# Performance work log

Measured on AMD Instinct MI355X. Metric: run time of the kernel, lower is better.

The kernel has to match this reference:

```python
import jax, jax.numpy as jnp
from jax import lax
import numpy as np

# dims
B, S, IN, E = 2, 2048, 512, 1024
INNER = 2 * E              # mLSTM up-projection, proj_factor = 2.0
NH = 4                     # mLSTM cell heads
DH = INNER // NH           # 512
QKV_BLK = 4                # qkv_proj_blocksize
NHW = INNER // QKV_BLK     # heads of block-diagonal (headwise) q/k/v projections
K = 4                      # causal conv1d kernel size
EPS = 1e-6                 # mLSTM cell eps
LN_EPS = 1e-5


def setup_inputs() -> dict:
    key = jax.random.key(0)
    ks = jax.random.split(key, 16)
    n = lambda k, shp, s=0.02: jax.random.normal(k, shp, jnp.float32) * s
    z = lambda shp: jnp.zeros(shp, jnp.float32)
    return dict(
        x=jax.random.normal(ks[0], (B, S, IN), jnp.float32),
        w_in=n(ks[1], (IN, E)), b_in=z((E,)),
        ln1_w=jnp.ones((E,), jnp.float32),
        w_up=n(ks[2], (E, 2 * INNER)), b_up=z((2 * INNER,)),
        conv_w=n(ks[3], (INNER, K), 0.1), conv_b=z((INNER,)),
        q_w=n(ks[4], (NHW, QKV_BLK, QKV_BLK), 0.3), q_b=z((INNER,)),
        k_w=n(ks[5], (NHW, QKV_BLK, QKV_BLK), 0.3), k_b=z((INNER,)),
        v_w=n(ks[6], (NHW, QKV_BLK, QKV_BLK), 0.3), v_b=z((INNER,)),
        ig_w=n(ks[7], (3 * INNER, NH)), ig_b=z((NH,)),
        fg_w=n(ks[8], (3 * INNER, NH)), fg_b=jnp.ones((NH,), jnp.float32),
        onorm_w=jnp.ones((INNER,), jnp.float32),
        skip=n(ks[9], (INNER,), 1.0),
        w_down=n(ks[10], (INNER, E)), b_down=z((E,)),
        post_w=jnp.ones((E,), jnp.float32),
    )


def _layernorm(x, w, eps=LN_EPS):
    m = x.mean(-1, keepdims=True)
    v = x.var(-1, keepdims=True)
    return (x - m) / jnp.sqrt(v + eps) * w


def _headwise(x, w, b):
    # block-diagonal linear: x (B,S,INNER) split into NHW blocks of QKV_BLK
    Bx, Sx, _ = x.shape
    y = jnp.einsum('bshd,hod->bsho', x.reshape(Bx, Sx, NHW, QKV_BLK), w)
    return y.reshape(Bx, Sx, INNER) + b


def _mlstm_parallel(q, k, v, ig, fg):
    # q,k,v: (B,NH,S,DH); ig,fg: (B,NH,S). Parallel (stabilized) mLSTM.
    log_f = jax.nn.log_sigmoid(fg)                       # (B,NH,S)
    cum = jnp.cumsum(log_f, axis=-1)                     # inclusive cumsum
    dmat = cum[..., :, None] - cum[..., None, :]         # F_i - F_j  (B,NH,S,S)
    mask = jnp.tril(jnp.ones((S, S), bool))
    logD = jnp.where(mask, dmat + ig[..., None, :], -jnp.inf)
    m = logD.max(-1, keepdims=True)                      # (B,NH,S,1)
    Dm = jnp.exp(logD - m)
    qk = jnp.einsum('bnid,bnjd->bnij', q, k) / jnp.sqrt(jnp.float32(DH))
    C = qk * Dm
    norm = jnp.maximum(jnp.abs(C.sum(-1, keepdims=True)), jnp.exp(-m))
    return jnp.einsum('bnij,bnjd->bnid', C / (norm + EPS), v)


def _forward(x, w_in, b_in, ln1_w, w_up, b_up, conv_w, conv_b,
             q_w, q_b, k_w, k_b, v_w, v_b, ig_w, ig_b, fg_w, fg_b,
             onorm_w, skip, w_down, b_down, post_w):
    h_in = x @ w_in + b_in                               # (B,S,E); dropout = identity (eval)

    # --- mLSTM block: residual + pre-LN ---
    xn = _layernorm(h_in, ln1_w)
    up = xn @ w_up + b_up                                # (B,S,2*INNER)
    x_m, z = jnp.split(up, 2, axis=-1)

    # causal depthwise conv1d + SiLU
    rhs = conv_w.T[:, None, :]                           # (K,1,INNER)
    xc = lax.conv_general_dilated(x_m, rhs, window_strides=(1,),
                                  padding=[(K - 1, 0)],
                                  dimension_numbers=('NHC', 'HIO', 'NHC'),
                                  feature_group_count=INNER) + conv_b
    x_conv_act = jax.nn.silu(xc)

    q = _headwise(x_conv_act, q_w, q_b)                  # (B,S,INNER)
    k = _headwise(x_conv_act, k_w, k_b)
    v = _headwise(x_m, v_w, v_b)

    if_in = jnp.concatenate([q, k, v], axis=-1)          # (B,S,3*INNER)
    ig = (if_in @ ig_w + ig_b).transpose(0, 2, 1)        # (B,NH,S)
    fg = (if_in @ fg_w + fg_b).transpose(0, 2, 1)

    to_heads = lambda t: t.reshape(B, S, NH, DH).transpose(0, 2, 1, 3)
    h = _mlstm_parallel(to_heads(q), to_heads(k), to_heads(v), ig, fg)  # (B,NH,S,DH)

    # multi-head (group) norm over DH, then learned scale over flat features
    hn = (h - h.mean(-1, keepdims=True)) / jnp.sqrt(h.var(-1, keepdims=True) + LN_EPS)
    hn = hn.transpose(0, 2, 1, 3).reshape(B, S, INNER) * onorm_w

    h_skip = hn + skip * x_conv_act                      # learnable skip
    h_gated = h_skip * jax.nn.silu(z)                    # output gate
    y = h_gated @ w_down + b_down                        # (B,S,E)

    out = h_in + y                                       # residual
    return _layernorm(out, post_w)                       # post_blocks_norm


def reference(x, w_in, b_in, ln1_w, w_up, b_up, conv_w, conv_b,
              q_w, q_b, k_w, k_b, v_w, v_b, ig_w, ig_b, fg_w, fg_b,
              onorm_w, skip, w_down, b_down, post_w):
    return _forward(x, w_in, b_in, ln1_w, w_up, b_up, conv_w, conv_b,
                    q_w, q_b, k_w, k_b, v_w, v_b, ig_w, ig_b, fg_w, fg_b,
                    onorm_w, skip, w_down, b_down, post_w)
```

## Files before the change

kernel.cpp:

```cpp
#include <hip/hip_runtime.h>
#include <hip/hip_bf16.h>

typedef __hip_bfloat16 bf16;
typedef float floatx4 __attribute__((ext_vector_type(4)));
typedef short bf16x8 __attribute__((ext_vector_type(8)));

#define B_      2
#define S_      2048
#define IN_     512
#define E_      1024
#define INNER_  2048
#define NH_     4
#define DH_     512
#define T_      (B_*S_)
#define EPS_CELL 1e-6f
#define LN_EPS_  1e-5f
#define LS      72
#define CTB_    4

__device__ inline float b2f(bf16 x){ return __bfloat162float(x); }
__device__ inline bf16  f2b(float x){ return __float2bfloat16(x); }
__device__ inline float us2f(unsigned short u){ union{unsigned int i; float f;} v; v.i = ((unsigned int)u)<<16; return v.f; }
__device__ inline float u2f(unsigned int u){ union{unsigned int i; float f;} v; v.i = u; return v.f; }
__device__ inline unsigned short f2bu(float x){ bf16 t = __float2bfloat16(x); unsigned short r; __builtin_memcpy(&r,&t,2); return r; }
__device__ inline void unpack8(uint4 u, float* f){
  f[0]=u2f(u.x<<16); f[1]=u2f(u.x&0xffff0000u);
  f[2]=u2f(u.y<<16); f[3]=u2f(u.y&0xffff0000u);
  f[4]=u2f(u.z<<16); f[5]=u2f(u.z&0xffff0000u);
  f[6]=u2f(u.w<<16); f[7]=u2f(u.w&0xffff0000u);
}
__device__ inline uint4 pack8(const float* f){
  uint4 u;
  u.x = (unsigned)f2bu(f[0]) | ((unsigned)f2bu(f[1])<<16);
  u.y = (unsigned)f2bu(f[2]) | ((unsigned)f2bu(f[3])<<16);
  u.z = (unsigned)f2bu(f[4]) | ((unsigned)f2bu(f[5])<<16);
  u.w = (unsigned)f2bu(f[6]) | ((unsigned)f2bu(f[7])<<16);
  return u;
}
__device__ inline void stv(bf16* p, float v){ *p = f2b(v); }
__device__ inline void stv(float* p, float v){ *p = v; }

typedef __attribute__((address_space(3))) unsigned int lds_u32_t;
typedef __attribute__((address_space(1))) const unsigned int glb_u32_t;
__device__ __forceinline__ void cp_async16(const bf16* g, short* l){
  __builtin_amdgcn_global_load_lds((glb_u32_t*)(const void*)g,
                                   (lds_u32_t*)(void*)l, 16, 0, 0);
}
__device__ __forceinline__ int so_(int row, int c8){ return row*64 + (((c8) ^ (row&7))<<3); }
__device__ __forceinline__ int eo_(int row, int ch){ return row*128 + (((ch) ^ (row&15))<<3); }

#define STAGE_ASYNC(dst, srcbase, stride, kk) \
  { int slot_ = (kk)*256 + tid; int r_ = slot_>>3; int c8_ = (slot_&7) ^ (r_&7); \
    cp_async16((srcbase) + (size_t)r_*(stride) + c8_*8, &dst[slot_*8]); }

__global__ __launch_bounds__(256) void convert_bf16(const float* __restrict__ X,
    bf16* __restrict__ Y, int n8){
  int i = blockIdx.x*256 + threadIdx.x;
  if (i >= n8) return;
  const float4* p = (const float4*)(X) + i*2;
  float4 a = p[0], b = p[1];
  ushort4 o0, o1;
  o0.x=f2bu(a.x); o0.y=f2bu(a.y); o0.z=f2bu(a.z); o0.w=f2bu(a.w);
  o1.x=f2bu(b.x); o1.y=f2bu(b.y); o1.z=f2bu(b.z); o1.w=f2bu(b.w);
  ushort4* q = (ushort4*)(Y) + i*2;
  q[0]=o0; q[1]=o1;
}

__global__ __launch_bounds__(256) void transpose_conv_w(const float* __restrict__ W,
    bf16* __restrict__ Wt, int K, int N){
  int n0 = blockIdx.x*64, k0 = blockIdx.y*64;
  __shared__ float tl[64][65];
  int tid = threadIdx.x;
  #pragma unroll
  for (int i=0;i<4;i++){
    int idx = tid + i*256; int r = idx>>4, c4 = idx&15;
    float4 v = *(const float4*)(W + (size_t)(k0+r)*N + n0 + c4*4);
    tl[r][c4*4+0]=v.x; tl[r][c4*4+1]=v.y; tl[r][c4*4+2]=v.z; tl[r][c4*4+3]=v.w;
  }
  __syncthreads();
  #pragma unroll
  for (int i=0;i<4;i++){
    int idx = tid + i*256; int rn = idx>>4, c4 = idx&15;
    ushort4 o;
    o.x=f2bu(tl[c4*4+0][rn]); o.y=f2bu(tl[c4*4+1][rn]);
    o.z=f2bu(tl[c4*4+2][rn]); o.w=f2bu(tl[c4*4+3][rn]);
    *(ushort4*)(Wt + (size_t)(n0+rn)*K + k0 + c4*4) = o;
  }
}

__global__ __launch_bounds__(256) void mfma_gemm(const bf16* __restrict__ A,
    const bf16* __restrict__ Bt, const float* __restrict__ bias, bf16* __restrict__ C,
    int Kd, int lda, int ldc, int NN){
  int bid = blockIdx.x;
  int MM = gridDim.x / NN;
  int mPerX = MM >> 3;
  int xcd = bid & 7, seq = bid >> 3;
  int nb = seq % NN, mb = xcd*mPerX + seq / NN;
  int n0 = nb*128, m0 = mb*128;
  __shared__ __align__(16) short smem[128*128];
  short* As = smem;
  short* Bs = smem + 128*64;
  int tid = threadIdx.x;
  int w = tid>>6, l = tid&63, lq = l>>4, lr = l&15;
  int wm = (w>>1)*64, wn = (w&1)*64;
  const bf16* Abase = A + (size_t)m0*lda;
  const bf16* Bbase = Bt + (size_t)n0*Kd;
  floatx4 acc[4][4];
  #pragma unroll
  for (int mi=0;mi<4;mi++){
    #pragma unroll
    for (int ni=0;ni<4;ni++) acc[mi][ni] = (floatx4){0.f,0.f,0.f,0.f};
  }
  for (int k0=0; k0<Kd; k0+=64){
    __syncthreads();
    #pragma unroll
    for (int kk=0;kk<4;kk++){
      STAGE_ASYNC(As, Abase + k0, lda, kk);
      STAGE_ASYNC(Bs, Bbase + k0, Kd, kk);
    }
    __syncthreads();
    #pragma unroll
    for (int ks=0; ks<2; ks++){
      bf16x8 af[4], bfr[4];
      #pragma unroll
      for (int mi=0;mi<4;mi++) af[mi] = *(const bf16x8*)&As[so_(wm+mi*16+lr, ks*4+lq)];
      #pragma unroll
      for (int ni=0;ni<4;ni++) bfr[ni] = *(const bf16x8*)&Bs[so_(wn+ni*16+lr, ks*4+lq)];
      #pragma unroll
      for (int mi=0;mi<4;mi++){
        #pragma unroll
        for (int ni=0;ni<4;ni++)
          acc[mi][ni] = __builtin_amdgcn_mfma_f32_16x16x32_bf16(af[mi], bfr[ni], acc[mi][ni], 0,0,0);
      }
    }
  }
  float bb[4];
  #pragma unroll
  for (int ni=0;ni<4;ni++) bb[ni] = bias[n0 + wn + ni*16 + lr];
  __syncthreads();
  #pragma unroll
  for (int mi=0;mi<4;mi++){
    #pragma unroll
    for (int ni=0;ni<4;ni++){
      int coll = wn + ni*16 + lr;
      int ch = coll>>3, off = coll&7;
      #pragma unroll
      for (int r=0;r<4;r++){
        int rowl = wm + mi*16 + lq*4 + r;
        smem[rowl*128 + (((ch) ^ (rowl&15))<<3) + off] = (short)f2bu(acc[mi][ni][r] + bb[ni]);
      }
    }
  }
  __syncthreads();
  #pragma unroll
  for (int i=0;i<8;i++){
    int slot = i*256 + tid;
    int r = slot >> 4, c8 = slot & 15;
    uint4 val = *(const uint4*)&smem[eo_(r, c8)];
    *(uint4*)(C + (size_t)(m0+r)*ldc + n0 + c8*8) = val;
  }
}

template<typename OutT>
__global__ __launch_bounds__(256) void ln_rows(const bf16* __restrict__ X,
    const bf16* __restrict__ Xadd, const float* __restrict__ w, OutT* __restrict__ Y){
  int row = blockIdx.x, tid = threadIdx.x;
  size_t base = (size_t)row*E_;
  float vals[4], s=0.f, s2=0.f;
  #pragma unroll
  for (int e=0;e<4;e++){
    int c = e*256+tid;
    float v = b2f(X[base+c]);
    if (Xadd) v += b2f(Xadd[base+c]);
    vals[e]=v; s+=v; s2+=v*v;
  }
  __shared__ float sa[256], sb[256];
  sa[tid]=s; sb[tid]=s2; __syncthreads();
  for (int off=128; off>0; off>>=1){
    if (tid<off){ sa[tid]+=sa[tid+off]; sb[tid]+=sb[tid+off]; }
    __syncthreads();
  }
  float mean = sa[0]*(1.f/E_);
  float var  = sb[0]*(1.f/E_) - mean*mean;
  float rstd = rsqrtf(var + LN_EPS_);
  #pragma unroll
  for (int e=0;e<4;e++){
    int c = e*256+tid;
    stv(&Y[base+c], (vals[e]-mean)*rstd*w[c]);
  }
}

__global__ __launch_bounds__(256) void conv_headwise(const bf16* __restrict__ up,
    const float* __restrict__ cw, const float* __restrict__ cb,
    const float* __restrict__ qw, const float* __restrict__ qb,
    const float* __restrict__ kw, const float* __restrict__ kb,
    const float* __restrict__ vw, const float* __restrict__ vb,
    bf16* __restrict__ xca, bf16* __restrict__ q, bf16* __restrict__ k,
    bf16* __restrict__ v){
  int t0 = blockIdx.x*CTB_;
  int s0 = t0 & (S_-1);
  int c0 = threadIdx.x*8;
  int hw0 = c0 >> 2;

  float row[7][8];
  #pragma unroll
  for (int j=0;j<7;j++){
    if (s0-3+j >= 0){
      uint4 rv = *(const uint4*)(up + (size_t)(t0-3+j)*(2*INNER_) + c0);
      unpack8(rv, row[j]);
    } else {
      #pragma unroll
      for (int e=0;e<8;e++) row[j][e]=0.f;
    }
  }

  float xc[CTB_][8];
  {
    float cwv[8][4], cbv[8];
    #pragma unroll
    for (int e=0;e<8;e++){
      float4 w4 = *(const float4*)(cw + (size_t)(c0+e)*4);
      cwv[e][0]=w4.x; cwv[e][1]=w4.y; cwv[e][2]=w4.z; cwv[e][3]=w4.w;
    }
    float4 b0 = *(const float4*)(cb+c0), b1 = *(const float4*)(cb+c0+4);
    cbv[0]=b0.x; cbv[1]=b0.y; cbv[2]=b0.z; cbv[3]=b0.w;
    cbv[4]=b1.x; cbv[5]=b1.y; cbv[6]=b1.z; cbv[7]=b1.w;
    #pragma unroll
    for (int i=0;i<CTB_;i++){
      #pragma unroll
      for (int e=0;e<8;e++){
        float a = cbv[e];
        #pragma unroll
        for (int t=0;t<4;t++) a += row[i+t][e]*cwv[e][t];
        xc[i][e] = a/(1.f+expf(-a));
      }
      *(uint4*)(xca + (size_t)(t0+i)*INNER_ + c0) = pack8(xc[i]);
    }
  }

  {
    float wv_[32], bv[8];
    #pragma unroll
    for (int g=0;g<2;g++){
      #pragma unroll
      for (int r4=0;r4<4;r4++){
        float4 w4 = *(const float4*)(vw + (size_t)(hw0+g)*16 + r4*4);
        wv_[g*16+r4*4+0]=w4.x; wv_[g*16+r4*4+1]=w4.y;
        wv_[g*16+r4*4+2]=w4.z; wv_[g*16+r4*4+3]=w4.w;
      }
    }
    float4 b0 = *(const float4*)(vb+c0), b1 = *(const float4*)(vb+c0+4);
    bv[0]=b0.x; bv[1]=b0.y; bv[2]=b0.z; bv[3]=b0.w;
    bv[4]=b1.x; bv[5]=b1.y; bv[6]=b1.z; bv[7]=b1.w;
    #pragma unroll
    for (int i=0;i<CTB_;i++){
      float ov[8];
      #pragma unroll
      for (int g=0;g<2;g++){
        #pragma unroll
        for (int o=0;o<4;o++){
          float a = bv[g*4+o];
          #pragma unroll
          for (int d=0;d<4;d++) a += row[i+3][g*4+d]*wv_[g*16+o*4+d];
          ov[g*4+o]=a;
        }
      }
      *(uint4*)(v + (size_t)(t0+i)*INNER_ + c0) = pack8(ov);
    }
  }

  {
    float wv_[32], bv[8];
    #pragma unroll
    for (int g=0;g<2;g++){
      #pragma unroll
      for (int r4=0;r4<4;r4++){
        float4 w4 = *(const float4*)(qw + (size_t)(hw0+g)*16 + r4*4);
        wv_[g*16+r4*4+0]=w4.x; wv_[g*16+r4*4+1]=w4.y;
        wv_[g*16+r4*4+2]=w4.z; wv_[g*16+r4*4+3]=w4.w;
      }
    }
    float4 b0 = *(const float4*)(qb+c0), b1 = *(const float4*)(qb+c0+4);
    bv[0]=b0.x; bv[1]=b0.y; bv[2]=b0.z; bv[3]=b0.w;
    bv[4]=b1.x; bv[5]=b1.y; bv[6]=b1.z; bv[7]=b1.w;
    #pragma unroll
    for (int i=0;i<CTB_;i++){
      float ov[8];
      #pragma unroll
      for (int g=0;g<2;g++){
        #pragma unroll
        for (int o=0;o<4;o++){
          float a = bv[g*4+o];
          #pragma unroll
          for (int d=0;d<4;d++) a += xc[i][g*4+d]*wv_[g*16+o*4+d];
          ov[g*4+o]=a;
        }
      }
      *(uint4*)(q + (size_t)(t0+i)*INNER_ + c0) = pack8(ov);
    }
  }

  {
    float wv_[32], bv[8];
    #pragma unroll
    for (int g=0;g<2;g++){
      #pragma unroll
      for (int r4=0;r4<4;r4++){
        float4 w4 = *(const float4*)(kw + (size_t)(hw0+g)*16 + r4*4);
        wv_[g*16+r4*4+0]=w4.x; wv_[g*16+r4*4+1]=w4.y;
        wv_[g*16+r4*4+2]=w4.z; wv_[g*16+r4*4+3]=w4.w;
      }
    }
    float4 b0 = *(const float4*)(kb+c0), b1 = *(const float4*)(kb+c0+4);
    bv[0]=b0.x; bv[1]=b0.y; bv[2]=b0.z; bv[3]=b0.w;
    bv[4]=b1.x; bv[5]=b1.y; bv[6]=b1.z; bv[7]=b1.w;
    #pragma unroll
    for (int i=0;i<CTB_;i++){
      float ov[8];
      #pragma unroll
      for (int g=0;g<2;g++){
        #pragma unroll
        for (int o=0;o<4;o++){
          float a = bv[g*4+o];
          #pragma unroll
          for (int d=0;d<4;d++) a += xc[i][g*4+d]*wv_[g*16+o*4+d];
          ov[g*4+o]=a;
        }
      }
      *(uint4*)(k + (size_t)(t0+i)*INNER_ + c0) = pack8(ov);
    }
  }
}

__global__ __launch_bounds__(256) void pack_gates_w(const float* __restrict__ igw,
    const float* __restrict__ fgw, bf16* __restrict__ gwb){
  int idx = blockIdx.x*256 + threadIdx.x;
  if (idx >= 3*INNER_) return;
  int g = idx >> 9;
  int e = (idx >> 6) & 7;
  int l = idx & 63;
  int r = g*512 + l*8 + e;
  float4 a = *(const float4*)(igw + (size_t)r*4);
  float4 b = *(const float4*)(fgw + (size_t)r*4);
  ushort4 o0, o1;
  o0.x=f2bu(a.x); o0.y=f2bu(a.y); o0.z=f2bu(a.z); o0.w=f2bu(a.w);
  o1.x=f2bu(b.x); o1.y=f2bu(b.y); o1.z=f2bu(b.z); o1.w=f2bu(b.w);
  *(ushort4*)(gwb + (size_t)idx*8)     = o0;
  *(ushort4*)(gwb + (size_t)idx*8 + 4) = o1;
}

__global__ __launch_bounds__(256) void gates_kernel(const bf16* __restrict__ q,
    const bf16* __restrict__ k, const bf16* __restrict__ v,
    const bf16* __restrict__ gwb, const float* __restrict__ igb,
    const float* __restrict__ fgb, float* __restrict__ igo, float* __restrict__ fgo){
  __shared__ float red[4*32];
  int tid = threadIdx.x;
  int w = tid >> 6, l = tid & 63;
  int quad = w >> 1, kh = w & 1;
  int tok0 = blockIdx.x*8 + quad*4;
  float acc[4][8];
  #pragma unroll
  for (int t=0;t<4;t++){
    #pragma unroll
    for (int n=0;n<8;n++) acc[t][n]=0.f;
  }
  #pragma unroll 2
  for (int it=0; it<6; ++it){
    int src = it >> 1, j = it & 1;
    const bf16* sp = (src==0) ? q : ((src==1) ? k : v);
    int pos = kh*1024 + j*512 + l*8;
    int g = src*4 + kh*2 + j;
    uint4 dv[4];
    #pragma unroll
    for (int t=0;t<4;t++)
      dv[t] = *(const uint4*)(sp + (size_t)(tok0+t)*INNER_ + pos);
    float d[4][8];
    #pragma unroll
    for (int t=0;t<4;t++) unpack8(dv[t], d[t]);
    const bf16* wb = gwb + (size_t)g*512*8;
    #pragma unroll
    for (int e=0;e<8;e++){
      uint4 wv = *(const uint4*)(wb + (size_t)(e*64 + l)*8);
      float w8[8]; unpack8(wv, w8);
      #pragma unroll
      for (int t=0;t<4;t++){
        #pragma unroll
        for (int n=0;n<8;n++) acc[t][n] += d[t][e]*w8[n];
      }
    }
  }
  #pragma unroll
  for (int off=1; off<64; off<<=1){
    #pragma unroll
    for (int t=0;t<4;t++){
      #pragma unroll
      for (int n=0;n<8;n++) acc[t][n] += __shfl_xor(acc[t][n], off);
    }
  }
  if (l == 0){
    #pragma unroll
    for (int t=0;t<4;t++){
      #pragma unroll
      for (int n=0;n<8;n++) red[w*32 + t*8 + n] = acc[t][n];
    }
  }
  __syncthreads();
  if (tid < 64){
    int qd = tid >> 5, tn = tid & 31;
    int t = tn >> 3, n = tn & 7;
    float val = red[(qd*2)*32 + tn] + red[(qd*2+1)*32 + tn];
    int tok = blockIdx.x*8 + qd*4 + t;
    int b = tok >> 11, s = tok & (S_-1);
    if (n < 4) igo[((size_t)(b*NH_+n))*S_ + s] = val + igb[n];
    else       fgo[((size_t)(b*NH_+(n-4)))*S_ + s] = val + fgb[n-4];
  }
}

__global__ __launch_bounds__(256) void scan8(const float* __restrict__ igp,
    const float* __restrict__ fgp, float* __restrict__ ap,
    float* __restrict__ Mp, float* __restrict__ flp, float* __restrict__ rowsum){
  int h = blockIdx.x, tid = threadIdx.x;
  const float* fg = fgp + (size_t)h*S_;
  const float* ig = igp + (size_t)h*S_;
  int base = tid*8;
  float loc[8], run = 0.f;
  #pragma unroll
  for (int e=0;e<8;e++){
    float x = fg[base+e];
    float ls = fminf(x,0.f) - log1pf(expf(-fabsf(x)));
    run += ls; loc[e] = run;
  }
  __shared__ float sd[256];
  sd[tid]=run; __syncthreads();
  if (tid==0){ float r=0.f; for(int t=0;t<256;t++){ float t0=sd[t]; sd[t]=r; r+=t0; } }
  __syncthreads();
  float off = sd[tid];
  float lm[8], rm = -3e38f;
  #pragma unroll
  for (int e=0;e<8;e++){
    float F = loc[e]+off; loc[e]=F;
    float aj = ig[base+e]-F;
    ap[(size_t)h*S_+base+e]=aj;
    rm = fmaxf(rm, aj); lm[e]=rm;
  }
  __syncthreads();
  sd[tid]=rm; __syncthreads();
  if (tid==0){ float r=-3e38f; for(int t=0;t<256;t++){ float t0=sd[t]; sd[t]=r; r=fmaxf(r,t0); } }
  __syncthreads();
  float offm = sd[tid];
  #pragma unroll
  for (int e=0;e<8;e++){
    float M = fmaxf(lm[e], offm);
    Mp[(size_t)h*S_+base+e]=M;
    flp[(size_t)h*S_+base+e]=expf(-loc[e]-M);
    rowsum[(size_t)h*S_+base+e]=0.f;
  }
}

__global__ __launch_bounds__(256) void transpose_v(const bf16* __restrict__ v,
    bf16* __restrict__ vT){
  int sb = blockIdx.x, db = blockIdx.y, h = blockIdx.z;
  int b = h >> 2, n = h & 3;
  int s0 = sb*64, d0 = db*64;
  __shared__ short tl[64*LS];
  int tid = threadIdx.x;
  #pragma unroll
  for (int i=0;i<2;i++){
    int vv = tid + i*256; int r = vv>>3, c8 = vv&7;
    uint4 x = *(const uint4*)(v + (size_t)(b*S_+s0+r)*INNER_ + n*DH_ + d0 + c8*8);
    *(uint4*)&tl[r*LS + c8*8] = x;
  }
  __syncthreads();
  #pragma unroll
  for (int i=0;i<2;i++){
    int vv = tid + i*256; int r = vv>>3, c8 = vv&7;
    unsigned short tmp[8];
    #pragma unroll
    for (int e=0;e<8;e++) tmp[e] = (unsigned short)tl[(c8*8+e)*LS + r];
    uint4 o; __builtin_memcpy(&o, tmp, 16);
    *(uint4*)(vT + ((size_t)h*DH_ + d0 + r)*S_ + s0 + c8*8) = o;
  }
}

__global__ __launch_bounds__(256) void qk_decay_kernel(const bf16* __restrict__ qg,
    const bf16* __restrict__ kg, const float* __restrict__ ap,
    const float* __restrict__ Mp, float* __restrict__ rowsum, bf16* __restrict__ W){
  int h = blockIdx.x & 7;
  int t = 271 - (blockIdx.x >> 3);
  int p = (int)((sqrtf(4.f*t+1.f)-1.f)*0.5f);
  while ((p+1)*(p+2) <= t) p++;
  while (p*(p+1) > t) p--;
  int r0 = t - p*(p+1);
  int nj = p + 1;
  int it = 2*p + (r0 >= nj ? 1 : 0);
  int tj = r0 >= nj ? r0 - nj : r0;
  int b = h >> 2, n = h & 3;
  int i0 = it*64, j0 = tj*128;
  __shared__ __align__(16) short smem[64*64 + 128*64];
  short* Qs = smem;
  short* Ks = smem + 64*64;
  __shared__ float a_s[128], m_s[64];
  int tid = threadIdx.x;
  if (tid < 128) a_s[tid] = ap[(size_t)h*S_ + j0 + tid];
  if (tid < 64)  m_s[tid] = Mp[(size_t)h*S_ + i0 + tid];
  int w = tid>>6, l = tid&63, lq = l>>4, lr = l&15;
  int wm = (w>>1)*32, wn = (w&1)*64;
  const bf16* Qbase = qg + (size_t)(b*S_+i0)*INNER_ + n*DH_;
  const bf16* Kbase = kg + (size_t)(b*S_+j0)*INNER_ + n*DH_;
  floatx4 acc[2][4];
  #pragma unroll
  for (int mi=0;mi<2;mi++){
    #pragma unroll
    for (int ni=0;ni<4;ni++) acc[mi][ni] = (floatx4){0.f,0.f,0.f,0.f};
  }
  for (int d0=0; d0<DH_; d0+=64){
    __syncthreads();
    STAGE_ASYNC(Qs, Qbase + d0, INNER_, 0);
    STAGE_ASYNC(Qs, Qbase + d0, INNER_, 1);
    #pragma unroll
    for (int kk=0;kk<4;kk++){
      STAGE_ASYNC(Ks, Kbase + d0, INNER_, kk);
    }
    __syncthreads();
    #pragma unroll
    for (int ks=0; ks<2; ks++){
      bf16x8 af[2], bfr[4];
      #pragma unroll
      for (int mi=0;mi<2;mi++) af[mi] = *(const bf16x8*)&Qs[so_(wm+mi*16+lr, ks*4+lq)];
      #pragma unroll
      for (int ni=0;ni<4;ni++) bfr[ni] = *(const bf16x8*)&Ks[so_(wn+ni*16+lr, ks*4+lq)];
      #pragma unroll
      for (int mi=0;mi<2;mi++){
        #pragma unroll
        for (int ni=0;ni<4;ni++)
          acc[mi][ni] = __builtin_amdgcn_mfma_f32_16x16x32_bf16(af[mi], bfr[ni], acc[mi][ni], 0,0,0);
      }
    }
  }
  const float scale = 0.04419417382415922f;
  float rpart[2][4];
  #pragma unroll
  for (int mi=0;mi<2;mi++){
    #pragma unroll
    for (int r=0;r<4;r++) rpart[mi][r]=0.f;
  }
  __syncthreads();
  #pragma unroll
  for (int mi=0;mi<2;mi++){
    #pragma unroll
    for (int ni=0;ni<4;ni++){
      int coll = wn + ni*16 + lr;
      int ch = coll>>3, off = coll&7;
      float av = a_s[coll];
      #pragma unroll
      for (int r=0;r<4;r++){
        int rowl = wm + mi*16 + lq*4 + r;
        int gi = i0 + rowl, gj = j0 + coll;
        float wv = 0.f;
        if (gj <= gi) wv = acc[mi][ni][r]*scale*__expf(av-m_s[rowl]);
        smem[rowl*128 + (((ch) ^ (rowl&15))<<3) + off] = (short)f2bu(wv);
        rpart[mi][r] += wv;
      }
    }
  }
  __syncthreads();
  #pragma unroll
  for (int i=0;i<4;i++){
    int slot = i*256 + tid;
    int r = slot >> 4, c8 = slot & 15;
    uint4 val = *(const uint4*)&smem[eo_(r, c8)];
    *(uint4*)(W + ((size_t)h*S_ + i0 + r)*S_ + j0 + c8*8) = val;
  }
  #pragma unroll
  for (int mi=0;mi<2;mi++){
    #pragma unroll
    for (int r=0;r<4;r++){
      float v = rpart[mi][r];
      v += __shfl_xor(v, 1, 16);
      v += __shfl_xor(v, 2, 16);
      v += __shfl_xor(v, 4, 16);
      v += __shfl_xor(v, 8, 16);
      if (lr == 0)
        atomicAdd(&rowsum[(size_t)h*S_ + i0 + wm + mi*16 + lq*4 + r], v);
    }
  }
}

__global__ __launch_bounds__(256) void pv_kernel(const bf16* __restrict__ W,
    const bf16* __restrict__ vT, const float* __restrict__ rowsum,
    const float* __restrict__ fl, bf16* __restrict__ O){
  int h = blockIdx.x & 7;
  int s = blockIdx.x >> 3;
  int ti = 31 - (s >> 2), tn = s & 3;
  int b = h >> 2, n = h & 3;
  int i0 = ti*64, d0 = tn*128;
  __shared__ __align__(16) short smem[64*64 + 128*64];
  short* Ws = smem;
  short* Vs = smem + 64*64;
  __shared__ float inv_s[64];
  int tid = threadIdx.x;
  if (tid < 64){
    size_t o = (size_t)h*S_ + i0 + tid;
    inv_s[tid] = 1.f/(fmaxf(fabsf(rowsum[o]), fl[o]) + EPS_CELL);
  }
  int w = tid>>6, l = tid&63, lq = l>>4, lr = l&15;
  int wm = (w>>1)*32, wn = (w&1)*64;
  const bf16* Wbase = W + ((size_t)h*S_ + i0)*S_;
  const bf16* Vbase = vT + ((size_t)h*DH_ + d0)*S_;
  floatx4 acc[2][4];
  #pragma unroll
  for (int mi=0;mi<2;mi++){
    #pragma unroll
    for (int ni=0;ni<4;ni++) acc[mi][ni] = (floatx4){0.f,0.f,0.f,0.f};
  }
  int jmax = i0 + 64;
  for (int j0=0; j0<jmax; j0+=64){
    __syncthreads();
    STAGE_ASYNC(Ws, Wbase + j0, S_, 0);
    STAGE_ASYNC(Ws, Wbase + j0, S_, 1);
    #pragma unroll
    for (int kk=0;kk<4;kk++){
      STAGE_ASYNC(Vs, Vbase + j0, S_, kk);
    }
    __syncthreads();
    #pragma unroll
    for (int ks=0; ks<2; ks++){
      bf16x8 af[2], bfr[4];
      #pragma unroll
      for (int mi=0;mi<2;mi++) af[mi] = *(const bf16x8*)&Ws[so_(wm+mi*16+lr, ks*4+lq)];
      #pragma unroll
      for (int ni=0;ni<4;ni++) bfr[ni] = *(const bf16x8*)&Vs[so_(wn+ni*16+lr, ks*4+lq)];
      #pragma unroll
      for (int mi=0;mi<2;mi++){
        #pragma unroll
        for (int ni=0;ni<4;ni++)
          acc[mi][ni] = __builtin_amdgcn_mfma_f32_16x16x32_bf16(af[mi], bfr[ni], acc[mi][ni], 0,0,0);
      }
    }
  }
  __syncthreads();
  #pragma unroll
  for (int mi=0;mi<2;mi++){
    #pragma unroll
    for (int ni=0;ni<4;ni++){
      int dl = wn + ni*16 + lr;
      int ch = dl>>3, off = dl&7;
      #pragma unroll
      for (int r=0;r<4;r++){
        int rowl = wm + mi*16 + lq*4 + r;
        smem[rowl*128 + (((ch) ^ (rowl&15))<<3) + off] = (short)f2bu(acc[mi][ni][r] * inv_s[rowl]);
      }
    }
  }
  __syncthreads();
  #pragma unroll
  for (int i=0;i<4;i++){
    int slot = i*256 + tid;
    int r = slot >> 4, c8 = slot & 15;
    uint4 val = *(const uint4*)&smem[eo_(r, c8)];
    *(uint4*)(O + (size_t)(b*S_ + i0 + r)*INNER_ + n*DH_ + d0 + c8*8) = val;
  }
}

__global__ __launch_bounds__(256) void headnorm_gate(const bf16* __restrict__ h,
    const float* __restrict__ onw, const float* __restrict__ skip,
    const bf16* __restrict__ xca, bf16* __restrict__ up){
  int bid = blockIdx.x;
  int n = bid & 3; int bs = bid >> 2;
  int tid = threadIdx.x;
  size_t hbase = (size_t)bs*INNER_ + n*DH_;
  float v0 = b2f(h[hbase+tid]);
  float v1 = b2f(h[hbase+256+tid]);
  __shared__ float sa[256], sb[256];
  sa[tid]=v0+v1; sb[tid]=v0*v0+v1*v1;
  __syncthreads();
  for (int off=128; off>0; off>>=1){
    if (tid<off){ sa[tid]+=sa[tid+off]; sb[tid]+=sb[tid+off]; }
    __syncthreads();
  }
  float mean = sa[0]*(1.f/DH_);
  float var  = sb[0]*(1.f/DH_) - mean*mean;
  float rstd = rsqrtf(var + LN_EPS_);
  #pragma unroll
  for (int e=0;e<2;e++){
    int dl = e*256+tid; int c = n*DH_+dl;
    float hv = e ? v1 : v0;
    float hn = (hv-mean)*rstd*onw[c];
    float hs = hn + skip[c]*b2f(xca[(size_t)bs*INNER_+c]);
    size_t zoff = (size_t)bs*(2*INNER_) + INNER_ + c;
    float zv = b2f(up[zoff]);
    float sz = zv/(1.f+expf(-zv));
    up[zoff] = f2b(hs*sz);
  }
}

extern "C" void kernel_launch(void* const* d_in, const int* in_sizes, int n_in,
                              void* d_out, int out_size, void* d_ws, size_t ws_size,
                              hipStream_t stream) {
  const float* x      = (const float*)d_in[0];
  const float* w_in   = (const float*)d_in[1];
  const float* b_in   = (const float*)d_in[2];
  const float* ln1_w  = (const float*)d_in[3];
  const float* w_up   = (const float*)d_in[4];
  const float* b_up   = (const float*)d_in[5];
  const float* conv_w = (const float*)d_in[6];
  const float* conv_b = (const float*)d_in[7];
  const float* q_w    = (const float*)d_in[8];
  const float* q_b    = (const float*)d_in[9];
  const float* k_w    = (const float*)d_in[10];
  const float* k_b    = (const float*)d_in[11];
  const float* v_w    = (const float*)d_in[12];
  const float* v_b    = (const float*)d_in[13];
  const float* ig_w   = (const float*)d_in[14];
  const float* ig_b   = (const float*)d_in[15];
  const float* fg_w   = (const float*)d_in[16];
  const float* fg_b   = (const float*)d_in[17];
  const float* onw    = (const float*)d_in[18];
  const float* skip   = (const float*)d_in[19];
  const float* w_down = (const float*)d_in[20];
  const float* b_down = (const float*)d_in[21];
  const float* post_w = (const float*)d_in[22];

  char* p = (char*)d_ws;
  auto alloc = [&](size_t bytes)->void*{ void* r = p; p += (bytes + 255) & ~(size_t)255; return r; };
  bf16* h_in = (bf16*)alloc((size_t)T_*E_*2);
  bf16* xn   = (bf16*)alloc((size_t)T_*E_*2);
  bf16* up   = (bf16*)alloc((size_t)T_*2*INNER_*2);
  bf16* xca  = (bf16*)alloc((size_t)T_*INNER_*2);
  bf16* qb_  = (bf16*)alloc((size_t)T_*INNER_*2);
  bf16* kb_  = (bf16*)alloc((size_t)T_*INNER_*2);
  bf16* vb_  = (bf16*)alloc((size_t)T_*INNER_*2);
  bf16* hb_  = (bf16*)alloc((size_t)T_*INNER_*2);
  float* igbuf = (float*)alloc((size_t)B_*NH_*S_*4);
  float* fgbuf = (float*)alloc((size_t)B_*NH_*S_*4);
  float* abuf  = (float*)alloc((size_t)B_*NH_*S_*4);
  float* Mbuf  = (float*)alloc((size_t)B_*NH_*S_*4);
  float* flbuf = (float*)alloc((size_t)B_*NH_*S_*4);
  float* rsbuf = (float*)alloc((size_t)B_*NH_*S_*4);
  bf16* gwb  = (bf16*)alloc((size_t)3*INNER_*8*2);
  bf16* Wbuf = (bf16*)alloc((size_t)B_*NH_*S_*S_*2);
  bf16* ybuf = xn;
  bf16* vTb  = hb_;
  bf16* obuf = vb_;
  bf16* xbf    = Wbuf;
  bf16* w_in_t = Wbuf + (size_t)T_*IN_;
  bf16* w_up_t = w_in_t + (size_t)E_*IN_;
  bf16* w_down_t = Wbuf;

  convert_bf16<<<(T_*IN_/8+255)/256, 256, 0, stream>>>(x, xbf, T_*IN_/8);
  transpose_conv_w<<<dim3(E_/64, IN_/64), 256, 0, stream>>>(w_in, w_in_t, IN_, E_);
  transpose_conv_w<<<dim3((2*INNER_)/64, E_/64), 256, 0, stream>>>(w_up, w_up_t, E_, 2*INNER_);
  pack_gates_w<<<(3*INNER_+255)/256, 256, 0, stream>>>(ig_w, fg_w, gwb);
  mfma_gemm<<<(T_/128)*(E_/128), 256, 0, stream>>>(xbf, w_in_t, b_in, h_in, IN_, IN_, E_, E_/128);
  ln_rows<bf16><<<T_, 256, 0, stream>>>(h_in, nullptr, ln1_w, xn);
  mfma_gemm<<<(T_/128)*((2*INNER_)/128), 256, 0, stream>>>(xn, w_up_t, b_up, up, E_, E_, 2*INNER_, (2*INNER_)/128);
  conv_headwise<<<T_/CTB_, 256, 0, stream>>>(up, conv_w, conv_b,
      q_w, q_b, k_w, k_b, v_w, v_b, xca, qb_, kb_, vb_);
  gates_kernel<<<T_/8, 256, 0, stream>>>(qb_, kb_, vb_, gwb, ig_b, fg_b, igbuf, fgbuf);
  scan8<<<B_*NH_, 256, 0, stream>>>(igbuf, fgbuf, abuf, Mbuf, flbuf, rsbuf);
  transpose_v<<<dim3(S_/64, DH_/64, B_*NH_), 256, 0, stream>>>(vb_, vTb);
  qk_decay_kernel<<<8*272, 256, 0, stream>>>(qb_, kb_, abuf, Mbuf, rsbuf, Wbuf);
  pv_kernel<<<8*128, 256, 0, stream>>>(Wbuf, vTb, rsbuf, flbuf, obuf);
  headnorm_gate<<<T_*NH_, 256, 0, stream>>>(obuf, onw, skip, xca, up);
  transpose_conv_w<<<dim3(E_/64, INNER_/64), 256, 0, stream>>>(w_down, w_down_t, INNER_, E_);
  mfma_gemm<<<(T_/128)*(E_/128), 256, 0, stream>>>(up + INNER_, w_down_t, b_down, ybuf, INNER_, 2*INNER_, E_, E_/128);
  ln_rows<float><<<T_, 256, 0, stream>>>(h_in, ybuf, post_w, (float*)d_out);
}
```

Before: 416.0 us.

## Double-buffer shared-memory tiles in GEMM, QK-decay and PV kernels

Switches the main GEMM, qk_decay and pv kernels from a single LDS buffer to two ping-pong buffers. The next K/D/J tile is prefetched asynchronously while MFMAs run on the current tile, and each iteration now needs one barrier instead of two. This is meant to hide global-load latency behind compute. In exchange, LDS use per block doubles (64KB for the GEMM), which may cut occupancy, and correctness depends on STAGE_ASYNC waiting properly before the barrier.

```diff
diff --git a/kernel.cpp b/kernel.cpp
--- a/kernel.cpp
+++ b/kernel.cpp
@@ -97,9 +97,7 @@
   int xcd = bid & 7, seq = bid >> 3;
   int nb = seq % NN, mb = xcd*mPerX + seq / NN;
   int n0 = nb*128, m0 = mb*128;
-  __shared__ __align__(16) short smem[128*128];
-  short* As = smem;
-  short* Bs = smem + 128*64;
+  __shared__ __align__(16) short smem[32768];
   int tid = threadIdx.x;
   int w = tid>>6, l = tid&63, lq = l>>4, lr = l&15;
   int wm = (w>>1)*64, wn = (w&1)*64;
@@ -111,14 +109,28 @@
     #pragma unroll
     for (int ni=0;ni<4;ni++) acc[mi][ni] = (floatx4){0.f,0.f,0.f,0.f};
   }
-  for (int k0=0; k0<Kd; k0+=64){
-    __syncthreads();
-    #pragma unroll
-    for (int kk=0;kk<4;kk++){
-      STAGE_ASYNC(As, Abase + k0, lda, kk);
-      STAGE_ASYNC(Bs, Bbase + k0, Kd, kk);
-    }
-    __syncthreads();
+  short* As0 = smem;          short* Bs0 = smem + 8192;
+  short* As1 = smem + 16384;  short* Bs1 = smem + 24576;
+  int NT = Kd >> 6;
+  #pragma unroll
+  for (int kk=0;kk<4;kk++){
+    STAGE_ASYNC(As0, Abase, lda, kk);
+    STAGE_ASYNC(Bs0, Bbase, Kd, kk);
+  }
+  __syncthreads();
+  for (int t=0; t<NT; ++t){
+    short* As  = (t&1) ? As1 : As0;
+    short* Bs  = (t&1) ? Bs1 : Bs0;
+    short* Asn = (t&1) ? As0 : As1;
+    short* Bsn = (t&1) ? Bs0 : Bs1;
+    if (t+1 < NT){
+      int k0 = (t+1)*64;
+      #pragma unroll
+      for (int kk=0;kk<4;kk++){
+        STAGE_ASYNC(Asn, Abase + k0, lda, kk);
+        STAGE_ASYNC(Bsn, Bbase + k0, Kd, kk);
+      }
+    }
     #pragma unroll
     for (int ks=0; ks<2; ks++){
       bf16x8 af[4], bfr[4];
@@ -133,11 +145,11 @@
           acc[mi][ni] = __builtin_amdgcn_mfma_f32_16x16x32_bf16(af[mi], bfr[ni], acc[mi][ni], 0,0,0);
       }
     }
+    __syncthreads();
   }
   float bb[4];
   #pragma unroll
   for (int ni=0;ni<4;ni++) bb[ni] = bias[n0 + wn + ni*16 + lr];
-  __syncthreads();
   #pragma unroll
   for (int mi=0;mi<4;mi++){
     #pragma unroll
@@ -496,9 +508,7 @@
   int tj = r0 >= nj ? r0 - nj : r0;
   int b = h >> 2, n = h & 3;
   int i0 = it*64, j0 = tj*128;
-  __shared__ __align__(16) short smem[64*64 + 128*64];
-  short* Qs = smem;
-  short* Ks = smem + 64*64;
+  __shared__ __align__(16) short smem[2*12288];
   __shared__ float a_s[128], m_s[64];
   int tid = threadIdx.x;
   if (tid < 128) a_s[tid] = ap[(size_t)h*S_ + j0 + tid];
@@ -513,15 +523,26 @@
     #pragma unroll
     for (int ni=0;ni<4;ni++) acc[mi][ni] = (floatx4){0.f,0.f,0.f,0.f};
   }
-  for (int d0=0; d0<DH_; d0+=64){
-    __syncthreads();
-    STAGE_ASYNC(Qs, Qbase + d0, INNER_, 0);
-    STAGE_ASYNC(Qs, Qbase + d0, INNER_, 1);
-    #pragma unroll
-    for (int kk=0;kk<4;kk++){
-      STAGE_ASYNC(Ks, Kbase + d0, INNER_, kk);
-    }
-    __syncthreads();
+  short* Qs0 = smem;          short* Ks0 = smem + 4096;
+  short* Qs1 = smem + 12288;  short* Ks1 = smem + 16384;
+  STAGE_ASYNC(Qs0, Qbase, INNER_, 0);
+  STAGE_ASYNC(Qs0, Qbase, INNER_, 1);
+  #pragma unroll
+  for (int kk=0;kk<4;kk++){ STAGE_ASYNC(Ks0, Kbase, INNER_, kk); }
+  __syncthreads();
+  const int NT = DH_/64;
+  for (int tt=0; tt<NT; ++tt){
+    short* Qs  = (tt&1) ? Qs1 : Qs0;
+    short* Ks  = (tt&1) ? Ks1 : Ks0;
+    short* Qsn = (tt&1) ? Qs0 : Qs1;
+    short* Ksn = (tt&1) ? Ks0 : Ks1;
+    if (tt+1 < NT){
+      int d0 = (tt+1)*64;
+      STAGE_ASYNC(Qsn, Qbase + d0, INNER_, 0);
+      STAGE_ASYNC(Qsn, Qbase + d0, INNER_, 1);
+      #pragma unroll
+      for (int kk=0;kk<4;kk++){ STAGE_ASYNC(Ksn, Kbase + d0, INNER_, kk); }
+    }
     #pragma unroll
     for (int ks=0; ks<2; ks++){
       bf16x8 af[2], bfr[4];
@@ -536,6 +557,7 @@
           acc[mi][ni] = __builtin_amdgcn_mfma_f32_16x16x32_bf16(af[mi], bfr[ni], acc[mi][ni], 0,0,0);
       }
     }
+    __syncthreads();
   }
   const float scale = 0.04419417382415922f;
   float rpart[2][4];
@@ -544,7 +566,6 @@
     #pragma unroll
     for (int r=0;r<4;r++) rpart[mi][r]=0.f;
   }
-  __syncthreads();
   #pragma unroll
   for (int mi=0;mi<2;mi++){
     #pragma unroll
@@ -594,9 +615,7 @@
   int ti = 31 - (s >> 2), tn = s & 3;
   int b = h >> 2, n = h & 3;
   int i0 = ti*64, d0 = tn*128;
-  __shared__ __align__(16) short smem[64*64 + 128*64];
-  short* Ws = smem;
-  short* Vs = smem + 64*64;
+  __shared__ __align__(16) short smem[2*12288];
   __shared__ float inv_s[64];
   int tid = threadIdx.x;
   if (tid < 64){
@@ -613,16 +632,26 @@
     #pragma unroll
     for (int ni=0;ni<4;ni++) acc[mi][ni] = (floatx4){0.f,0.f,0.f,0.f};
   }
-  int jmax = i0 + 64;
-  for (int j0=0; j0<jmax; j0+=64){
-    __syncthreads();
-    STAGE_ASYNC(Ws, Wbase + j0, S_, 0);
-    STAGE_ASYNC(Ws, Wbase + j0, S_, 1);
-    #pragma unroll
-    for (int kk=0;kk<4;kk++){
-      STAGE_ASYNC(Vs, Vbase + j0, S_, kk);
-    }
-    __syncthreads();
+  short* Ws0 = smem;          short* Vs0 = smem + 4096;
+  short* Ws1 = smem + 12288;  short* Vs1 = smem + 16384;
+  int NT = (i0 >> 6) + 1;
+  STAGE_ASYNC(Ws0, Wbase, S_, 0);
+  STAGE_ASYNC(Ws0, Wbase, S_, 1);
+  #pragma unroll
+  for (int kk=0;kk<4;kk++){ STAGE_ASYNC(Vs0, Vbase, S_, kk); }
+  __syncthreads();
+  for (int tt=0; tt<NT; ++tt){
+    short* Ws  = (tt&1) ? Ws1 : Ws0;
+    short* Vs  = (tt&1) ? Vs1 : Vs0;
+    short* Wsn = (tt&1) ? Ws0 : Ws1;
+    short* Vsn = (tt&1) ? Vs0 : Vs1;
+    if (tt+1 < NT){
+      int j0 = (tt+1)*64;
+      STAGE_ASYNC(Wsn, Wbase + j0, S_, 0);
+      STAGE_ASYNC(Wsn, Wbase + j0, S_, 1);
+      #pragma unroll
+      for (int kk=0;kk<4;kk++){ STAGE_ASYNC(Vsn, Vbase + j0, S_, kk); }
+    }
     #pragma unroll
     for (int ks=0; ks<2; ks++){
       bf16x8 af[2], bfr[4];
@@ -637,8 +666,8 @@
           acc[mi][ni] = __builtin_amdgcn_mfma_f32_16x16x32_bf16(af[mi], bfr[ni], acc[mi][ni], 0,0,0);
       }
     }
-  }
-  __syncthreads();
+    __syncthreads();
+  }
   #pragma unroll
   for (int mi=0;mi<2;mi++){
     #pragma unroll
```

Result: faster. 377.5 us (-9.2%).
